# Optimization experiments

Measured on AMD Instinct MI355X. Metric: run time of the kernel, lower is better.

## Reference

```python
import jax, jax.numpy as jnp
import numpy as np

B = 16384      # batch
T = 14         # number of embedding tables
L = 100000     # rows per table (table has L+1 rows due to the +1 offset)
E = 16         # em_size
H = 50         # user click history length


def setup_inputs() -> dict:
    key = jax.random.key(0)
    ks = jax.random.split(key, 10)
    sparse_features = jax.random.randint(ks[0], (B, T), 0, L, dtype=jnp.int32)
    dense_features = jax.random.normal(ks[1], (B, 1), dtype=jnp.float32)
    user_click_history = jax.random.randint(ks[2], (B, H), 0, L, dtype=jnp.int32)
    # stacked EmbeddingBag weights: [T, L+1, E]
    W = jax.random.normal(ks[3], (T, L + 1, E), dtype=jnp.float32) * 0.01
    fc1_w = jax.random.normal(ks[4], (200, 241), dtype=jnp.float32) / np.sqrt(241).astype(np.float32)
    fc1_b = jnp.zeros((200,), jnp.float32)
    fc2_w = jax.random.normal(ks[5], (80, 200), dtype=jnp.float32) / np.sqrt(200).astype(np.float32)
    fc2_b = jnp.zeros((80,), jnp.float32)
    fc3_w = jax.random.normal(ks[6], (2, 80), dtype=jnp.float32) / np.sqrt(80).astype(np.float32)
    fc3_b = jnp.zeros((2,), jnp.float32)
    return dict(sparse_features=sparse_features, dense_features=dense_features,
                user_click_history=user_click_history, W=W,
                fc1_w=fc1_w, fc1_b=fc1_b, fc2_w=fc2_w, fc2_b=fc2_b,
                fc3_w=fc3_w, fc3_b=fc3_b)


def reference(sparse_features, dense_features, user_click_history, W,
              fc1_w, fc1_b, fc2_w, fc2_b, fc3_w, fc3_b):
    # Per-table single-index EmbeddingBag(sum) == plain lookup. Batched gather
    # across all T tables at once: [B, T, E]
    embs = W[jnp.arange(T)[None, :], sparse_features + 1]
    embs = embs.reshape(embs.shape[0], T * E)  # [B, T*E]
    # tables[0].weight row 0 is zeroed before the history lookup (padding row).
    W0 = W[0].at[0].set(0.0)
    hist = W0[user_click_history + 1].sum(axis=1)  # [B, E] EmbeddingBag sum
    x = jnp.concatenate([embs, hist, dense_features], axis=1)  # [B, 241]
    x = jax.nn.relu(x @ fc1_w.T + fc1_b)
    x = jax.nn.relu(x @ fc2_w.T + fc2_b)
    return x @ fc3_w.T + fc3_b  # [B, 2]
```

## Files before the change

### kernel.cpp

```cpp
#include <hip/hip_runtime.h>


using u16 = unsigned short;
typedef __attribute__((ext_vector_type(8))) short short8v;
typedef __attribute__((ext_vector_type(4))) short short4v;
typedef __attribute__((ext_vector_type(4))) float floatx4;

constexpr int W1_ELEMS = 13 * 8 * 64 * 8;
constexpr int W2_ELEMS = 5 * 7 * 64 * 8;
constexpr int EF_ELEMS = 1024 * 7 * 64 * 8;
constexpr int HS_ELEMS = 1024 * 1024;

__device__ __forceinline__ u16 f2bf(float f) {
  unsigned u = __float_as_uint(f);
  unsigned r = (u + 0x7fffu + ((u >> 16) & 1u)) >> 16;
  return (u16)r;
}
__device__ __forceinline__ float bf2f(u16 h) {
  return __uint_as_float(((unsigned)h) << 16);
}

__global__ __launch_bounds__(256) void prep_kernel(
    const float* __restrict__ w1, const float* __restrict__ w2,
    const float* __restrict__ W, const int* __restrict__ sf,
    const int* __restrict__ hist, const float* __restrict__ dense,
    u16* __restrict__ w1h, u16* __restrict__ w2h,
    u16* __restrict__ ef, u16* __restrict__ hs) {
  const int b = blockIdx.x;
  const int tix = threadIdx.x;
  short8v z8 = {0, 0, 0, 0, 0, 0, 0, 0};

  if (b < 35) {
    int tid = b * 256 + tix;
    if (tid < 13 * 8 * 64) {
      int l = tid & 63;
      int g = tid >> 6;
      int kt = g & 7, nt = g >> 3;
      int n = nt * 16 + (l & 15);
      int kb = kt * 32 + (l >> 4) * 8;
      short8v h8;
#pragma unroll
      for (int e = 0; e < 8; ++e) {
        int k = kb + e;
        float v = (n < 200 && k < 241) ? w1[n * 241 + k] : 0.f;
        h8[e] = (short)f2bf(v);
      }
      *(short8v*)&w1h[tid * 8] = h8;
    } else if (tid < 13 * 8 * 64 + 5 * 7 * 64) {
      int t2 = tid - 13 * 8 * 64;
      int l = t2 & 63;
      int g = t2 >> 6;
      int kt = g % 7, nt = g / 7;
      int n = nt * 16 + (l & 15);
      int kb = kt * 32 + (l >> 4) * 8;
      short8v h8;
#pragma unroll
      for (int e = 0; e < 8; ++e) {
        int k = kb + e;
        float v = (k < 200) ? w2[n * 200 + k] : 0.f;
        h8[e] = (short)f2bf(v);
      }
      *(short8v*)&w2h[t2 * 8] = h8;
    }
  } else if (b < 3619) {
    int g = (b - 35) * 256 + tix;
    int t = g >> 16;
    int bb = (g >> 2) & 16383;
    int q = g & 3;
    int idx = sf[bb * 14 + t] + 1;
    floatx4 v4 = *(const floatx4*)(W + ((size_t)t * 100001 + (size_t)idx) * 16 + q * 4);
    short4v h4;
#pragma unroll
    for (int d = 0; d < 4; ++d) h4[d] = (short)f2bf(v4[d]);
    int k0 = t * 16 + q * 4;
    int kt = k0 >> 5, kg = (k0 >> 3) & 3, e0 = k0 & 7;
    int tile = bb >> 4, r = bb & 15;
    *(short4v*)&ef[((tile * 7 + kt) * 64 + kg * 16 + r) * 8 + e0] = h4;
  } else {
    int tile = b - 3619;
    int row0 = tile * 16;
    int r = tix >> 4, rem = tix & 15, q = rem & 3, s = rem >> 2;
    const int* hp = hist + (row0 + r) * 50;
    float a0 = 0.f, a1 = 0.f, a2 = 0.f, a3 = 0.f;
#pragma unroll
    for (int hh = 0; hh < 12; ++hh) {
      int idx = hp[s + hh * 4] + 1;
      floatx4 p = *(const floatx4*)(W + (size_t)idx * 16 + q * 4);
      a0 += p[0];
      a1 += p[1];
      a2 += p[2];
      a3 += p[3];
    }
    if (s < 2) {
      int idx = hp[48 + s] + 1;
      floatx4 p = *(const floatx4*)(W + (size_t)idx * 16 + q * 4);
      a0 += p[0];
      a1 += p[1];
      a2 += p[2];
      a3 += p[3];
    }
    a0 += __shfl_xor(a0, 4);
    a1 += __shfl_xor(a1, 4);
    a2 += __shfl_xor(a2, 4);
    a3 += __shfl_xor(a3, 4);
    a0 += __shfl_xor(a0, 8);
    a1 += __shfl_xor(a1, 8);
    a2 += __shfl_xor(a2, 8);
    a3 += __shfl_xor(a3, 8);
    if (s == 0) {
      float vals[4] = {a0, a1, a2, a3};
      short4v h4, l4;
#pragma unroll
      for (int d = 0; d < 4; ++d) {
        u16 hi = f2bf(vals[d]);
        h4[d] = (short)hi;
        l4[d] = (short)f2bf(vals[d] - bf2f(hi));
      }
      u16* ht = hs + (size_t)tile * 1024;
      int base = ((q >> 1) * 16 + r) * 8 + ((q * 4) & 7);
      *(short4v*)&ht[base] = h4;
      *(short4v*)&ht[512 + base] = l4;
      if (q == 0) {
        float dv = dense[row0 + r];
        u16 dh = f2bf(dv), dl = f2bf(dv - bf2f(dh));
        short8v dh8 = z8, dl8 = z8;
        dh8[0] = (short)dh;
        dl8[0] = (short)dl;
        *(short8v*)&ht[(32 + r) * 8] = dh8;
        *(short8v*)&ht[512 + (32 + r) * 8] = dl8;
        *(short8v*)&ht[(48 + r) * 8] = z8;
        *(short8v*)&ht[512 + (48 + r) * 8] = z8;
      }
    }
  }
}

__global__ __launch_bounds__(256, 1) void mlp_kernel(
    const u16* __restrict__ ef, const u16* __restrict__ hs,
    const u16* __restrict__ w1h, const u16* __restrict__ w2h,
    const float* __restrict__ b1, const float* __restrict__ b2,
    const float* __restrict__ w3, const float* __restrict__ b3,
    float* __restrict__ out) {
  __shared__ u16 A2h[4 * 7 * 64 * 8], A2l[4 * 7 * 64 * 8];
  __shared__ float o2[64 * 84];

  const int tid = threadIdx.x;
  const int l = tid & 63;
  const int wv = tid >> 6;
  const int blk = blockIdx.x;
  const int row0 = blk * 64;
  short8v z8 = {0, 0, 0, 0, 0, 0, 0, 0};
  const int ntbase = (wv == 0) ? 0 : 4 + 3 * (wv - 1);
  const int ntcnt = (wv == 0) ? 4 : 3;

  short8v a7h[4], a7l[4];
#pragma unroll
  for (int sub = 0; sub < 4; ++sub) {
    const u16* ht = hs + (size_t)(blk * 4 + sub) * 1024;
    a7h[sub] = *(const short8v*)&ht[l * 8];
    a7l[sub] = *(const short8v*)&ht[512 + l * 8];
  }
  short8v ga[2][4];
#pragma unroll
  for (int kk = 0; kk < 2; ++kk)
#pragma unroll
    for (int sub = 0; sub < 4; ++sub)
      ga[kk][sub] = *(const short8v*)&ef[(((blk * 4 + sub) * 7 + kk) * 64 + l) * 8];
  short8v bhr[2][4];
#pragma unroll
  for (int kk = 0; kk < 2; ++kk)
#pragma unroll
    for (int i = 0; i < 4; ++i)
      bhr[kk][i] = (i < ntcnt) ? *(const short8v*)&w1h[(((ntbase + i) * 8 + kk) * 64 + l) * 8]
                               : z8;

  floatx4 acc[4][4];
#pragma unroll
  for (int i = 0; i < 4; ++i)
#pragma unroll
    for (int sub = 0; sub < 4; ++sub) acc[i][sub] = (floatx4){0.f, 0.f, 0.f, 0.f};

#pragma unroll
  for (int kt = 0; kt < 8; ++kt) {
    const int cur = kt & 1;
    short8v a_[4];
#pragma unroll
    for (int sub = 0; sub < 4; ++sub) a_[sub] = (kt < 7) ? ga[cur][sub] : a7h[sub];
    if (kt < 5) {
#pragma unroll
      for (int sub = 0; sub < 4; ++sub)
        ga[cur][sub] = *(const short8v*)&ef[(((blk * 4 + sub) * 7 + kt + 2) * 64 + l) * 8];
    }
#pragma unroll
    for (int i = 0; i < 4; ++i) {
      if (i < ntcnt) {
        short8v cb = bhr[cur][i];
        if (kt < 6)
          bhr[cur][i] = *(const short8v*)&w1h[(((ntbase + i) * 8 + kt + 2) * 64 + l) * 8];
#pragma unroll
        for (int sub = 0; sub < 4; ++sub) {
          acc[i][sub] = __builtin_amdgcn_mfma_f32_16x16x32_bf16(a_[sub], cb, acc[i][sub], 0, 0, 0);
          if (kt == 7)
            acc[i][sub] = __builtin_amdgcn_mfma_f32_16x16x32_bf16(a7l[sub], cb, acc[i][sub], 0, 0, 0);
        }
      }
    }
  }

  const int ntA = wv;
  const bool dual = (wv == 1);
  short8v bra[2], brb[2];
  bra[0] = *(const short8v*)&w2h[((ntA * 7 + 0) * 64 + l) * 8];
  bra[1] = *(const short8v*)&w2h[((ntA * 7 + 1) * 64 + l) * 8];
  brb[0] = dual ? *(const short8v*)&w2h[((4 * 7 + 0) * 64 + l) * 8] : z8;
  brb[1] = dual ? *(const short8v*)&w2h[((4 * 7 + 1) * 64 + l) * 8] : z8;

#pragma unroll
  for (int i = 0; i < 4; ++i) {
    if (i < ntcnt) {
      int n = (ntbase + i) * 16 + (l & 15);
      float bias = (n < 200) ? b1[n] : 0.f;
      int kt2 = n >> 5, kg2 = (n >> 3) & 3, e = n & 7;
#pragma unroll
      for (int sub = 0; sub < 4; ++sub) {
#pragma unroll
        for (int g = 0; g < 4; ++g) {
          float v = (n < 200) ? fmaxf(acc[i][sub][g] + bias, 0.f) : 0.f;
          int m = (l >> 4) * 4 + g;
          u16 hi = f2bf(v), lo = f2bf(v - bf2f(hi));
          int pos = ((sub * 7 + kt2) * 64 + kg2 * 16 + m) * 8 + e;
          A2h[pos] = hi;
          A2l[pos] = lo;
        }
      }
    }
  }
  if (wv == 1 && l < 32) {
#pragma unroll
    for (int sub = 0; sub < 4; ++sub) {
      *(short8v*)&A2h[((sub * 7 + 6) * 64 + 32 + l) * 8] = z8;
      *(short8v*)&A2l[((sub * 7 + 6) * 64 + 32 + l) * 8] = z8;
    }
  }
  __syncthreads();

  floatx4 acc2a[4], acc2b[4];
#pragma unroll
  for (int sub = 0; sub < 4; ++sub) {
    acc2a[sub] = (floatx4){0.f, 0.f, 0.f, 0.f};
    acc2b[sub] = (floatx4){0.f, 0.f, 0.f, 0.f};
  }
#pragma unroll
  for (int kt = 0; kt < 7; ++kt) {
    short8v ca = bra[kt & 1];
    if (kt < 5) bra[kt & 1] = *(const short8v*)&w2h[((ntA * 7 + kt + 2) * 64 + l) * 8];
    short8v cb2 = brb[kt & 1];
    if (dual && kt < 5) brb[kt & 1] = *(const short8v*)&w2h[((4 * 7 + kt + 2) * 64 + l) * 8];
#pragma unroll
    for (int sub = 0; sub < 4; ++sub) {
      short8v ah = *(const short8v*)&A2h[((sub * 7 + kt) * 64 + l) * 8];
      short8v al = *(const short8v*)&A2l[((sub * 7 + kt) * 64 + l) * 8];
      acc2a[sub] = __builtin_amdgcn_mfma_f32_16x16x32_bf16(ah, ca, acc2a[sub], 0, 0, 0);
      acc2a[sub] = __builtin_amdgcn_mfma_f32_16x16x32_bf16(al, ca, acc2a[sub], 0, 0, 0);
      if (dual) {
        acc2b[sub] = __builtin_amdgcn_mfma_f32_16x16x32_bf16(ah, cb2, acc2b[sub], 0, 0, 0);
        acc2b[sub] = __builtin_amdgcn_mfma_f32_16x16x32_bf16(al, cb2, acc2b[sub], 0, 0, 0);
      }
    }
  }

  {
    int n = ntA * 16 + (l & 15);
    float bias = b2[n];
#pragma unroll
    for (int sub = 0; sub < 4; ++sub)
#pragma unroll
      for (int g = 0; g < 4; ++g) {
        int r2 = sub * 16 + (l >> 4) * 4 + g;
        o2[r2 * 84 + n] = fmaxf(acc2a[sub][g] + bias, 0.f);
      }
    if (dual) {
      int n2 = 64 + (l & 15);
      float bias2 = b2[n2];
#pragma unroll
      for (int sub = 0; sub < 4; ++sub)
#pragma unroll
        for (int g = 0; g < 4; ++g) {
          int r2 = sub * 16 + (l >> 4) * 4 + g;
          o2[r2 * 84 + n2] = fmaxf(acc2b[sub][g] + bias2, 0.f);
        }
    }
  }
  __syncthreads();

  if (tid < 128) {
    int r = tid >> 1, o = tid & 1;
    float a = b3[o];
    const float* orow = &o2[r * 84];
    const float* wrow = &w3[o * 80];
#pragma unroll
    for (int j = 0; j < 80; j += 4) {
      floatx4 xv = *(const floatx4*)&orow[j];
      floatx4 wv4 = *(const floatx4*)&wrow[j];
      a += xv[0] * wv4[0] + xv[1] * wv4[1] + xv[2] * wv4[2] + xv[3] * wv4[3];
    }
    out[(row0 + r) * 2 + o] = a;
  }
}

extern "C" void kernel_launch(void* const* d_in, const int* in_sizes, int n_in,
                              void* d_out, int out_size, void* d_ws, size_t ws_size,
                              hipStream_t stream) {
  const int* sf = (const int*)d_in[0];
  const float* dense = (const float*)d_in[1];
  const int* hist = (const int*)d_in[2];
  const float* W = (const float*)d_in[3];
  const float* w1 = (const float*)d_in[4];
  const float* b1 = (const float*)d_in[5];
  const float* w2 = (const float*)d_in[6];
  const float* b2 = (const float*)d_in[7];
  const float* w3 = (const float*)d_in[8];
  const float* b3 = (const float*)d_in[9];
  float* out = (float*)d_out;

  u16* w1h = (u16*)d_ws;
  u16* w2h = w1h + W1_ELEMS;
  u16* ef = w2h + W2_ELEMS;
  u16* hs = ef + EF_ELEMS;

  prep_kernel<<<dim3(35 + 3584 + 1024), dim3(256), 0, stream>>>(
      w1, w2, W, sf, hist, dense, w1h, w2h, ef, hs);
  mlp_kernel<<<dim3(256), dim3(256), 0, stream>>>(ef, hs, w1h, w2h, b1, b2, w3, b3, out);
}
```

Before: 37.02 us.

## Split MLP kernel work across 16 waves per block, one row tile per wave

The MLP kernel now runs 1024 threads per block instead of 256. Each wave handles a single 16-row sub-tile for its group of output column tiles, where before one wave looped over all four sub-tiles. This raises wave-level parallelism and latency hiding and cuts per-thread register use, at the cost of loading the W1/W2 fragments redundantly across four waves. Block-wide barriers are also inserted mid-loop to keep the waves in lockstep, which may add stalls.

After: 35.26 us. 4.7% less time.

```diff
diff --git a/kernel.cpp b/kernel.cpp
--- a/kernel.cpp
+++ b/kernel.cpp
@@ -9,7 +9,6 @@
 constexpr int W1_ELEMS = 13 * 8 * 64 * 8;
 constexpr int W2_ELEMS = 5 * 7 * 64 * 8;
 constexpr int EF_ELEMS = 1024 * 7 * 64 * 8;
-constexpr int HS_ELEMS = 1024 * 1024;
 
 __device__ __forceinline__ u16 f2bf(float f) {
   unsigned u = __float_as_uint(f);
@@ -135,7 +134,7 @@
   }
 }
 
-__global__ __launch_bounds__(256, 1) void mlp_kernel(
+__global__ __launch_bounds__(1024, 4) void mlp_kernel(
     const u16* __restrict__ ef, const u16* __restrict__ hs,
     const u16* __restrict__ w1h, const u16* __restrict__ w2h,
     const float* __restrict__ b1, const float* __restrict__ b2,
@@ -146,26 +145,24 @@
 
   const int tid = threadIdx.x;
   const int l = tid & 63;
-  const int wv = tid >> 6;
+  const int w = tid >> 6;
+  const int sub = w & 3;
+  const int ntg = w >> 2;
   const int blk = blockIdx.x;
+  const int tile = blk * 4 + sub;
   const int row0 = blk * 64;
   short8v z8 = {0, 0, 0, 0, 0, 0, 0, 0};
-  const int ntbase = (wv == 0) ? 0 : 4 + 3 * (wv - 1);
-  const int ntcnt = (wv == 0) ? 4 : 3;
-
-  short8v a7h[4], a7l[4];
-#pragma unroll
-  for (int sub = 0; sub < 4; ++sub) {
-    const u16* ht = hs + (size_t)(blk * 4 + sub) * 1024;
-    a7h[sub] = *(const short8v*)&ht[l * 8];
-    a7l[sub] = *(const short8v*)&ht[512 + l * 8];
-  }
-  short8v ga[2][4];
-#pragma unroll
-  for (int kk = 0; kk < 2; ++kk)
-#pragma unroll
-    for (int sub = 0; sub < 4; ++sub)
-      ga[kk][sub] = *(const short8v*)&ef[(((blk * 4 + sub) * 7 + kk) * 64 + l) * 8];
+  const int ntbase = (ntg == 0) ? 0 : 4 + 3 * (ntg - 1);
+  const int ntcnt = (ntg == 0) ? 4 : 3;
+
+  const u16* ht = hs + (size_t)tile * 1024;
+  short8v a7h = *(const short8v*)&ht[l * 8];
+  short8v a7l = *(const short8v*)&ht[512 + l * 8];
+
+  short8v ga[2];
+  ga[0] = *(const short8v*)&ef[((tile * 7 + 0) * 64 + l) * 8];
+  ga[1] = *(const short8v*)&ef[((tile * 7 + 1) * 64 + l) * 8];
+
   short8v bhr[2][4];
 #pragma unroll
   for (int kk = 0; kk < 2; ++kk)
@@ -174,44 +171,33 @@
       bhr[kk][i] = (i < ntcnt) ? *(const short8v*)&w1h[(((ntbase + i) * 8 + kk) * 64 + l) * 8]
                                : z8;
 
-  floatx4 acc[4][4];
-#pragma unroll
-  for (int i = 0; i < 4; ++i)
-#pragma unroll
-    for (int sub = 0; sub < 4; ++sub) acc[i][sub] = (floatx4){0.f, 0.f, 0.f, 0.f};
+  floatx4 acc[4];
+#pragma unroll
+  for (int i = 0; i < 4; ++i) acc[i] = (floatx4){0.f, 0.f, 0.f, 0.f};
 
 #pragma unroll
   for (int kt = 0; kt < 8; ++kt) {
     const int cur = kt & 1;
-    short8v a_[4];
-#pragma unroll
-    for (int sub = 0; sub < 4; ++sub) a_[sub] = (kt < 7) ? ga[cur][sub] : a7h[sub];
-    if (kt < 5) {
-#pragma unroll
-      for (int sub = 0; sub < 4; ++sub)
-        ga[cur][sub] = *(const short8v*)&ef[(((blk * 4 + sub) * 7 + kt + 2) * 64 + l) * 8];
-    }
+    short8v ah = (kt < 7) ? ga[cur] : a7h;
+    if (kt < 5) ga[cur] = *(const short8v*)&ef[((tile * 7 + kt + 2) * 64 + l) * 8];
 #pragma unroll
     for (int i = 0; i < 4; ++i) {
       if (i < ntcnt) {
         short8v cb = bhr[cur][i];
         if (kt < 6)
           bhr[cur][i] = *(const short8v*)&w1h[(((ntbase + i) * 8 + kt + 2) * 64 + l) * 8];
-#pragma unroll
-        for (int sub = 0; sub < 4; ++sub) {
-          acc[i][sub] = __builtin_amdgcn_mfma_f32_16x16x32_bf16(a_[sub], cb, acc[i][sub], 0, 0, 0);
-          if (kt == 7)
-            acc[i][sub] = __builtin_amdgcn_mfma_f32_16x16x32_bf16(a7l[sub], cb, acc[i][sub], 0, 0, 0);
-        }
-      }
-    }
-  }
-
-  const int ntA = wv;
-  const bool dual = (wv == 1);
+        acc[i] = __builtin_amdgcn_mfma_f32_16x16x32_bf16(ah, cb, acc[i], 0, 0, 0);
+        if (kt == 7)
+          acc[i] = __builtin_amdgcn_mfma_f32_16x16x32_bf16(a7l, cb, acc[i], 0, 0, 0);
+      }
+    }
+    if (kt == 2 || kt == 5) __builtin_amdgcn_s_barrier();
+  }
+
+  const bool dual = (ntg == 3);
   short8v bra[2], brb[2];
-  bra[0] = *(const short8v*)&w2h[((ntA * 7 + 0) * 64 + l) * 8];
-  bra[1] = *(const short8v*)&w2h[((ntA * 7 + 1) * 64 + l) * 8];
+  bra[0] = *(const short8v*)&w2h[((ntg * 7 + 0) * 64 + l) * 8];
+  bra[1] = *(const short8v*)&w2h[((ntg * 7 + 1) * 64 + l) * 8];
   brb[0] = dual ? *(const short8v*)&w2h[((4 * 7 + 0) * 64 + l) * 8] : z8;
   brb[1] = dual ? *(const short8v*)&w2h[((4 * 7 + 1) * 64 + l) * 8] : z8;
 
@@ -222,73 +208,56 @@
       float bias = (n < 200) ? b1[n] : 0.f;
       int kt2 = n >> 5, kg2 = (n >> 3) & 3, e = n & 7;
 #pragma unroll
-      for (int sub = 0; sub < 4; ++sub) {
-#pragma unroll
-        for (int g = 0; g < 4; ++g) {
-          float v = (n < 200) ? fmaxf(acc[i][sub][g] + bias, 0.f) : 0.f;
-          int m = (l >> 4) * 4 + g;
-          u16 hi = f2bf(v), lo = f2bf(v - bf2f(hi));
-          int pos = ((sub * 7 + kt2) * 64 + kg2 * 16 + m) * 8 + e;
-          A2h[pos] = hi;
-          A2l[pos] = lo;
-        }
-      }
-    }
-  }
-  if (wv == 1 && l < 32) {
-#pragma unroll
-    for (int sub = 0; sub < 4; ++sub) {
-      *(short8v*)&A2h[((sub * 7 + 6) * 64 + 32 + l) * 8] = z8;
-      *(short8v*)&A2l[((sub * 7 + 6) * 64 + 32 + l) * 8] = z8;
-    }
+      for (int g = 0; g < 4; ++g) {
+        float v = (n < 200) ? fmaxf(acc[i][g] + bias, 0.f) : 0.f;
+        int m = (l >> 4) * 4 + g;
+        u16 hi = f2bf(v), lo = f2bf(v - bf2f(hi));
+        int pos = ((sub * 7 + kt2) * 64 + kg2 * 16 + m) * 8 + e;
+        A2h[pos] = hi;
+        A2l[pos] = lo;
+      }
+    }
+  }
+  if (ntg == 1 && l < 32) {
+    *(short8v*)&A2h[((sub * 7 + 6) * 64 + 32 + l) * 8] = z8;
+    *(short8v*)&A2l[((sub * 7 + 6) * 64 + 32 + l) * 8] = z8;
   }
   __syncthreads();
 
-  floatx4 acc2a[4], acc2b[4];
-#pragma unroll
-  for (int sub = 0; sub < 4; ++sub) {
-    acc2a[sub] = (floatx4){0.f, 0.f, 0.f, 0.f};
-    acc2b[sub] = (floatx4){0.f, 0.f, 0.f, 0.f};
-  }
+  floatx4 acc2a = (floatx4){0.f, 0.f, 0.f, 0.f};
+  floatx4 acc2b = (floatx4){0.f, 0.f, 0.f, 0.f};
 #pragma unroll
   for (int kt = 0; kt < 7; ++kt) {
+    short8v ah = *(const short8v*)&A2h[((sub * 7 + kt) * 64 + l) * 8];
+    short8v al = *(const short8v*)&A2l[((sub * 7 + kt) * 64 + l) * 8];
     short8v ca = bra[kt & 1];
-    if (kt < 5) bra[kt & 1] = *(const short8v*)&w2h[((ntA * 7 + kt + 2) * 64 + l) * 8];
-    short8v cb2 = brb[kt & 1];
-    if (dual && kt < 5) brb[kt & 1] = *(const short8v*)&w2h[((4 * 7 + kt + 2) * 64 + l) * 8];
-#pragma unroll
-    for (int sub = 0; sub < 4; ++sub) {
-      short8v ah = *(const short8v*)&A2h[((sub * 7 + kt) * 64 + l) * 8];
-      short8v al = *(const short8v*)&A2l[((sub * 7 + kt) * 64 + l) * 8];
-      acc2a[sub] = __builtin_amdgcn_mfma_f32_16x16x32_bf16(ah, ca, acc2a[sub], 0, 0, 0);
-      acc2a[sub] = __builtin_amdgcn_mfma_f32_16x16x32_bf16(al, ca, acc2a[sub], 0, 0, 0);
-      if (dual) {
-        acc2b[sub] = __builtin_amdgcn_mfma_f32_16x16x32_bf16(ah, cb2, acc2b[sub], 0, 0, 0);
-        acc2b[sub] = __builtin_amdgcn_mfma_f32_16x16x32_bf16(al, cb2, acc2b[sub], 0, 0, 0);
-      }
+    if (kt < 5) bra[kt & 1] = *(const short8v*)&w2h[((ntg * 7 + kt + 2) * 64 + l) * 8];
+    acc2a = __builtin_amdgcn_mfma_f32_16x16x32_bf16(ah, ca, acc2a, 0, 0, 0);
+    acc2a = __builtin_amdgcn_mfma_f32_16x16x32_bf16(al, ca, acc2a, 0, 0, 0);
+    if (dual) {
+      short8v cb2 = brb[kt & 1];
+      if (kt < 5) brb[kt & 1] = *(const short8v*)&w2h[((4 * 7 + kt + 2) * 64 + l) * 8];
+      acc2b = __builtin_amdgcn_mfma_f32_16x16x32_bf16(ah, cb2, acc2b, 0, 0, 0);
+      acc2b = __builtin_amdgcn_mfma_f32_16x16x32_bf16(al, cb2, acc2b, 0, 0, 0);
     }
   }
 
   {
-    int n = ntA * 16 + (l & 15);
+    int n = ntg * 16 + (l & 15);
     float bias = b2[n];
 #pragma unroll
-    for (int sub = 0; sub < 4; ++sub)
-#pragma unroll
-      for (int g = 0; g < 4; ++g) {
-        int r2 = sub * 16 + (l >> 4) * 4 + g;
-        o2[r2 * 84 + n] = fmaxf(acc2a[sub][g] + bias, 0.f);
-      }
+    for (int g = 0; g < 4; ++g) {
+      int r2 = sub * 16 + (l >> 4) * 4 + g;
+      o2[r2 * 84 + n] = fmaxf(acc2a[g] + bias, 0.f);
+    }
     if (dual) {
       int n2 = 64 + (l & 15);
       float bias2 = b2[n2];
 #pragma unroll
-      for (int sub = 0; sub < 4; ++sub)
-#pragma unroll
-        for (int g = 0; g < 4; ++g) {
-          int r2 = sub * 16 + (l >> 4) * 4 + g;
-          o2[r2 * 84 + n2] = fmaxf(acc2b[sub][g] + bias2, 0.f);
-        }
+      for (int g = 0; g < 4; ++g) {
+        int r2 = sub * 16 + (l >> 4) * 4 + g;
+        o2[r2 * 84 + n2] = fmaxf(acc2b[g] + bias2, 0.f);
+      }
     }
   }
   __syncthreads();
@@ -330,5 +299,5 @@
 
   prep_kernel<<<dim3(35 + 3584 + 1024), dim3(256), 0, stream>>>(
       w1, w2, W, sf, hist, dense, w1h, w2h, ef, hs);
-  mlp_kernel<<<dim3(256), dim3(256), 0, stream>>>(ef, hs, w1h, w2h, b1, b2, w3, b3, out);
-}
+  mlp_kernel<<<dim3(256), dim3(1024), 0, stream>>>(ef, hs, w1h, w2h, b1, b2, w3, b3, out);
+}
```
